# Performance work log

Measured on AMD Instinct MI355X. Metric: run time of the kernel, lower is better.

The kernel has to match this reference:

```python
import jax, jax.numpy as jnp
from jax import lax
import numpy as np

H = 256      # encoder_hidden
F = 256      # variance predictor filter_size
K = 3        # kernel_size
NBINS = 256  # variance_embedding n_bins
B, S, T = 64, 512, 2048


def conv1d(x, w, b, pad):
    # x: [B, L, Cin], w: [K, Cin, Cout] -> [B, L, Cout]
    y = lax.conv_general_dilated(x, w, window_strides=(1,), padding=[(pad, pad)],
                                 dimension_numbers=('NWC', 'WIO', 'NWC'))
    return y + b


def layer_norm(x, g, b, eps=1e-5):
    mu = jnp.mean(x, -1, keepdims=True)
    v = jnp.mean((x - mu) ** 2, -1, keepdims=True)
    return (x - mu) * lax.rsqrt(v + eps) * g + b


def predictor(x, mask, w1, b1, g1, be1, w2, b2, g2, be2, lw, lb):
    h = jax.nn.relu(conv1d(x, w1, b1, (K - 1) // 2))
    h = layer_norm(h, g1, be1)
    h = jax.nn.relu(conv1d(h, w2, b2, 1))  # padding=1 hardcoded in original conv1d_2
    h = layer_norm(h, g2, be2)
    out = (h @ lw + lb)[..., 0]            # [B, L]
    return jnp.where(mask, 0.0, out)       # masked_fill(mask, 0.0)


def setup_inputs():
    key = jax.random.key(0)
    ks = jax.random.split(key, 16)
    inp = {
        'x': jax.random.normal(ks[0], (B, S, H), jnp.float32),
        'pitch_target': jax.random.normal(ks[1], (B, S), jnp.float32),
        'energy_target': jax.random.normal(ks[2], (B, S), jnp.float32),
        'src_mask': jnp.zeros((B, S), bool),
        'duration': jax.random.randint(ks[3], (B, S), 0, 4, jnp.int32),
        'max_len': T,
    }
    i = 4
    for p in ['d', 'p', 'e']:
        inp[p + '_w1'] = jax.random.normal(ks[i], (K, H, F), jnp.float32) * 0.05; i += 1
        inp[p + '_b1'] = jnp.zeros((F,), jnp.float32)
        inp[p + '_g1'] = jnp.ones((F,), jnp.float32)
        inp[p + '_be1'] = jnp.zeros((F,), jnp.float32)
        inp[p + '_w2'] = jax.random.normal(ks[i], (K, F, F), jnp.float32) * 0.05; i += 1
        inp[p + '_b2'] = jnp.zeros((F,), jnp.float32)
        inp[p + '_g2'] = jnp.ones((F,), jnp.float32)
        inp[p + '_be2'] = jnp.zeros((F,), jnp.float32)
        inp[p + '_lw'] = jax.random.normal(ks[i], (F, 1), jnp.float32) * 0.05; i += 1
        inp[p + '_lb'] = jnp.zeros((1,), jnp.float32)
    inp['p_table'] = jax.random.normal(ks[i], (NBINS, H), jnp.float32) * 0.02; i += 1
    inp['e_table'] = jax.random.normal(ks[i], (NBINS, H), jnp.float32) * 0.02
    return inp


def reference(x, pitch_target, energy_target, src_mask, duration, max_len,
              d_w1, d_b1, d_g1, d_be1, d_w2, d_b2, d_g2, d_be2, d_lw, d_lb,
              p_w1, p_b1, p_g1, p_be1, p_w2, p_b2, p_g2, p_be2, p_lw, p_lb,
              e_w1, e_b1, e_g1, e_be1, e_w2, e_b2, e_g2, e_be2, e_lw, e_lb,
              p_table, e_table):
    # linear-quantized bins over the data range (stats.json min/max -> [-2, 2] for randn data)
    bins = jnp.linspace(-2.0, 2.0, NBINS - 1, dtype=jnp.float32)

    log_d_pred = predictor(x, src_mask, d_w1, d_b1, d_g1, d_be1, d_w2, d_b2, d_g2, d_be2, d_lw, d_lb)

    # phoneme-level pitch (training path: target given -> embed bucketized target)
    p_pred = predictor(x, src_mask, p_w1, p_b1, p_g1, p_be1, p_w2, p_b2, p_g2, p_be2, p_lw, p_lb)
    p_emb = p_table[jnp.searchsorted(bins, pitch_target, side='left')]  # torch.bucketize(right=False)
    x = x + p_emb

    # phoneme-level energy (predictor runs on x AFTER pitch embedding, as in original)
    e_pred = predictor(x, src_mask, e_w1, e_b1, e_g1, e_be1, e_w2, e_b2, e_g2, e_be2, e_lw, e_lb)
    e_emb = e_table[jnp.searchsorted(bins, energy_target, side='left')]
    x = x + e_emb

    # Length regulation: expand phoneme i duration[b, i] times, pad to max_len.
    cum = jnp.cumsum(duration, axis=1)                 # [B, S]
    mel_len = cum[:, -1]                               # [B]
    frames = jnp.arange(max_len)                       # [T]
    # frame t maps to first phoneme i with cum[i] > t
    idx = jax.vmap(lambda c: jnp.searchsorted(c, frames, side='right'))(cum)  # [B, T]
    idx = jnp.minimum(idx, duration.shape[1] - 1)
    mel = jnp.take_along_axis(x, idx[:, :, None], axis=1)                     # [B, T, H]
    valid = frames[None, :] < mel_len[:, None]
    mel = jnp.where(valid[:, :, None], mel, 0.0)       # zero-pad beyond mel_len

    d_rounded = duration
    return (mel, p_pred, e_pred, log_d_pred, d_rounded, mel_len)
```

## Files before the change

kernel.cpp:

```cpp
#include <hip/hip_runtime.h>
#include <cstdint>
#include <cstddef>


#define HH 256
#define SS 512
#define BB 64
#define TT 2048

typedef __bf16 bf16;
typedef __attribute__((ext_vector_type(8))) __bf16 bf16x8;
typedef __attribute__((ext_vector_type(4))) __bf16 bf16x4;
typedef __attribute__((ext_vector_type(4))) float f32x4;

static constexpr size_t WSZ  = (size_t)3 * HH * HH;
static constexpr size_t H1SZ = (size_t)BB * SS * HH;

__device__ __forceinline__ int swz(int r, int c) { return (r * HH + c) ^ ((r & 7) << 3); }

__device__ __forceinline__ float edge_val(int j) {
    const float step = 4.0f / 254.0f;
    if (j == 254) return 2.0f;
    return __fadd_rn(-2.0f, __fmul_rn((float)j, step));
}
__device__ __forceinline__ int bucket256(float v) {
    int lo = 0, hi = 255;
    while (lo < hi) {
        int mid = (lo + hi) >> 1;
        if (edge_val(mid) < v) lo = mid + 1; else hi = mid;
    }
    return lo;
}

__global__ void wt_pack(const float* __restrict__ w0, const float* __restrict__ w1,
                        const float* __restrict__ w2, const float* __restrict__ w3,
                        const float* __restrict__ w4, const float* __restrict__ w5,
                        bf16* __restrict__ wp) {
    const int cv = blockIdx.x / 3, k = blockIdx.x % 3;
    const float* wsel[6] = {w0, w1, w2, w3, w4, w5};
    const float* wk = wsel[cv] + (size_t)k * HH * HH;
    bf16* o = wp + ((size_t)(cv * 3 + k)) * HH * HH;
    for (int fb = 0; fb < 16; ++fb) {
        #pragma unroll
        for (int h = 0; h < 2; ++h) {
            const int idx  = threadIdx.x + 256 * h;
            const int kcb  = idx >> 6, lane = idx & 63;
            const int f    = fb * 16 + (lane & 15);
            const int c0   = kcb * 32 + (lane >> 4) * 8;
            bf16x8 v;
            #pragma unroll
            for (int j = 0; j < 8; ++j) v[j] = (bf16)wk[(size_t)(c0 + j) * HH + f];
            *(bf16x8*)(o + (((size_t)fb * 8 + kcb) * 64 + lane) * 8) = v;
        }
    }
}

struct Args3 {
    const float* bias[3];
    const float* g[3];
    const float* be[3];
    const float* lw[3];
    const float* lb[3];
    float*       out[3];
};

template <bool LIN>
__global__ __launch_bounds__(256, 3) void conv_all(
    const void* __restrict__ in,
    const float* __restrict__ tab,
    const float* __restrict__ tgt,
    const bf16* __restrict__ wpk,
    Args3 args,
    bf16* __restrict__ h1out,
    const uint8_t* __restrict__ mask)
{
    __shared__ alignas(16) bf16 tile[66 * HH];
    __shared__ float red_s[64][4], red_q[64][4];
    __shared__ float ln_m[64], ln_r[64];
    __shared__ int remb[66];

    const int tid    = threadIdx.x;
    const int pred   = blockIdx.x >> 9;
    const int within = blockIdx.x & 511;
    const int b      = within >> 3;
    const int s0     = (within & 7) * 64;
    const bool emb   = (!LIN) && (pred == 2);

    if (emb) {
        if (tid < 66) {
            int s = s0 - 1 + tid;
            remb[tid] = (s >= 0 && s < SS) ? bucket256(tgt[b * SS + s]) : 0;
        }
        __syncthreads();
    }

    if (!LIN) {
        const float* inb = (const float*)in + (size_t)b * SS * HH;
        for (int idx = tid; idx < 66 * 64; idx += 256) {
            const int r = idx >> 6, c4 = (idx & 63) << 2;
            const int s = s0 - 1 + r;
            float4 v = make_float4(0.f, 0.f, 0.f, 0.f);
            if (s >= 0 && s < SS) {
                v = *(const float4*)(inb + (size_t)s * HH + c4);
                if (emb) {
                    const float4 tv = *(const float4*)(tab + (size_t)remb[r] * HH + c4);
                    v.x += tv.x; v.y += tv.y; v.z += tv.z; v.w += tv.w;
                }
            }
            bf16x4 bv = {(bf16)v.x, (bf16)v.y, (bf16)v.z, (bf16)v.w};
            *(bf16x4*)&tile[swz(r, c4)] = bv;
        }
    } else {
        const bf16* inb = (const bf16*)in + (size_t)pred * H1SZ + (size_t)b * SS * HH;
        for (int idx = tid; idx < 66 * 32; idx += 256) {
            const int r = idx >> 5, c8 = (idx & 31) << 3;
            const int s = s0 - 1 + r;
            bf16x8 v = {};
            if (s >= 0 && s < SS) v = *(const bf16x8*)(inb + (size_t)s * HH + c8);
            *(bf16x8*)&tile[swz(r, c8)] = v;
        }
    }
    __syncthreads();

    const int lane = tid & 63;
    const int wv   = tid >> 6;
    const int ln15 = lane & 15;
    const int g8   = (lane >> 4) << 3;

    const bf16* wt = wpk + (size_t)(pred * 2 + (LIN ? 1 : 0)) * WSZ;

    f32x4 acc[4][4];
    #pragma unroll
    for (int nf = 0; nf < 4; ++nf) {
        const float bv = args.bias[pred][wv * 64 + nf * 16 + ln15];
        #pragma unroll
        for (int mf = 0; mf < 4; ++mf) acc[mf][nf] = f32x4{bv, bv, bv, bv};
    }

    bf16x8 a0[4], b0[4], a1[4], b1[4];

#define LOADSTEP(A_, B_, T_) do {                                              \
    const int k_ = (T_) >> 3, kcb_ = (T_) & 7;                                 \
    const int kc_ = kcb_ << 5;                                                 \
    const int ar_ = ln15 + k_;                                                 \
    _Pragma("unroll")                                                          \
    for (int mf_ = 0; mf_ < 4; ++mf_)                                          \
        A_[mf_] = *(const bf16x8*)&tile[swz(16 * mf_ + ar_, kc_ + g8)];        \
    const bf16* bp_ = wt + ((((size_t)k_ * 16 + wv * 4) * 8 + kcb_) << 9)      \
                         + (size_t)lane * 8;                                   \
    _Pragma("unroll")                                                          \
    for (int nf_ = 0; nf_ < 4; ++nf_)                                          \
        B_[nf_] = *(const bf16x8*)(bp_ + ((size_t)nf_ << 12));                 \
} while (0)

#define MFMASTEP(A_, B_) do {                                                  \
    _Pragma("unroll")                                                          \
    for (int mf_ = 0; mf_ < 4; ++mf_)                                          \
        _Pragma("unroll")                                                      \
        for (int nf_ = 0; nf_ < 4; ++nf_)                                      \
            acc[mf_][nf_] = __builtin_amdgcn_mfma_f32_16x16x32_bf16(           \
                A_[mf_], B_[nf_], acc[mf_][nf_], 0, 0, 0);                     \
} while (0)

    LOADSTEP(a0, b0, 0);
    #pragma unroll 1
    for (int t2 = 0; t2 < 11; ++t2) {
        const int t = 2 * t2;
        LOADSTEP(a1, b1, t + 1);
        MFMASTEP(a0, b0);
        LOADSTEP(a0, b0, t + 2);
        MFMASTEP(a1, b1);
    }
    LOADSTEP(a1, b1, 23);
    MFMASTEP(a0, b0);
    MFMASTEP(a1, b1);

#undef LOADSTEP
#undef MFMASTEP

    #pragma unroll
    for (int mf = 0; mf < 4; ++mf)
        #pragma unroll
        for (int nf = 0; nf < 4; ++nf)
            #pragma unroll
            for (int i = 0; i < 4; ++i)
                acc[mf][nf][i] = fmaxf(acc[mf][nf][i], 0.f);

    #pragma unroll
    for (int mf = 0; mf < 4; ++mf) {
        #pragma unroll
        for (int i = 0; i < 4; ++i) {
            float s = acc[mf][0][i] + acc[mf][1][i] + acc[mf][2][i] + acc[mf][3][i];
            float q = acc[mf][0][i] * acc[mf][0][i] + acc[mf][1][i] * acc[mf][1][i] +
                      acc[mf][2][i] * acc[mf][2][i] + acc[mf][3][i] * acc[mf][3][i];
            #pragma unroll
            for (int off = 1; off < 16; off <<= 1) {
                s += __shfl_xor(s, off);
                q += __shfl_xor(q, off);
            }
            if (ln15 == 0) {
                const int row = 16 * mf + (lane >> 4) * 4 + i;
                red_s[row][wv] = s;
                red_q[row][wv] = q;
            }
        }
    }
    __syncthreads();
    if (tid < 64) {
        const float s = red_s[tid][0] + red_s[tid][1] + red_s[tid][2] + red_s[tid][3];
        const float q = red_q[tid][0] + red_q[tid][1] + red_q[tid][2] + red_q[tid][3];
        const float mean = s * (1.f / 256.f);
        const float var  = q * (1.f / 256.f) - mean * mean;
        ln_m[tid] = mean;
        ln_r[tid] = rsqrtf(var + 1e-5f);
    }
    __syncthreads();

    float gv[4], bev[4];
    #pragma unroll
    for (int nf = 0; nf < 4; ++nf) {
        const int col = wv * 64 + nf * 16 + ln15;
        gv[nf]  = args.g[pred][col];
        bev[nf] = args.be[pred][col];
    }

    if (!LIN) {
        bf16* ob = h1out + (size_t)pred * H1SZ + ((size_t)(b * SS + s0)) * HH;
        #pragma unroll
        for (int mf = 0; mf < 4; ++mf) {
            #pragma unroll
            for (int i = 0; i < 4; ++i) {
                const int row = 16 * mf + (lane >> 4) * 4 + i;
                const float mean = ln_m[row], rs = ln_r[row];
                #pragma unroll
                for (int nf = 0; nf < 4; ++nf) {
                    const float o = (acc[mf][nf][i] - mean) * rs * gv[nf] + bev[nf];
                    ob[(size_t)row * HH + wv * 64 + nf * 16 + ln15] = (bf16)o;
                }
            }
        }
    } else {
        float lwv[4];
        #pragma unroll
        for (int nf = 0; nf < 4; ++nf) lwv[nf] = args.lw[pred][wv * 64 + nf * 16 + ln15];
        const float lb0 = args.lb[pred][0];
        #pragma unroll
        for (int mf = 0; mf < 4; ++mf) {
            #pragma unroll
            for (int i = 0; i < 4; ++i) {
                const int row = 16 * mf + (lane >> 4) * 4 + i;
                const float mean = ln_m[row], rs = ln_r[row];
                float t = 0.f;
                #pragma unroll
                for (int nf = 0; nf < 4; ++nf)
                    t += ((acc[mf][nf][i] - mean) * rs * gv[nf] + bev[nf]) * lwv[nf];
                #pragma unroll
                for (int off = 1; off < 16; off <<= 1) t += __shfl_xor(t, off);
                if (ln15 == 0) red_s[row][wv] = t;
            }
        }
        __syncthreads();
        if (tid < 64) {
            const int gr = b * SS + s0 + tid;
            const float dv = red_s[tid][0] + red_s[tid][1] + red_s[tid][2] + red_s[tid][3] + lb0;
            args.out[pred][gr] = mask[gr] ? 0.f : dv;
        }
    }
}

__global__ void dur_kernel(const int* __restrict__ dur, int* __restrict__ idxb,
                           int* __restrict__ mli,
                           float* __restrict__ drnd, float* __restrict__ mlen) {
    __shared__ int sb[SS];
    const int b = blockIdx.x, t = threadIdx.x;
    const int v = dur[b * SS + t];
    drnd[b * SS + t] = (float)v;
    sb[t] = v;
    __syncthreads();
    for (int off = 1; off < SS; off <<= 1) {
        const int add = (t >= off) ? sb[t - off] : 0;
        __syncthreads();
        sb[t] += add;
        __syncthreads();
    }
    const int hi = sb[t];
    const int lo = hi - v;
    for (int j = lo; j < hi; ++j) idxb[b * TT + j] = t;
    if (t == SS - 1) { mlen[b] = (float)hi; mli[b] = hi; }
}

__global__ __launch_bounds__(256) void gather_kernel(
    const float* __restrict__ x,
    const float* __restrict__ ptab, const float* __restrict__ pt,
    const float* __restrict__ etab, const float* __restrict__ et,
    const int* __restrict__ idxb, const int* __restrict__ mli,
    float* __restrict__ mel)
{
    const int lane = threadIdx.x & 63;
    for (int row = blockIdx.x * 4 + (threadIdx.x >> 6); row < BB * TT; row += 4096 * 4) {
        const int b = row >> 11;
        const int t = row & (TT - 1);
        float4 v = make_float4(0.f, 0.f, 0.f, 0.f);
        if (t < mli[b]) {
            const int idx = idxb[row];
            const size_t src = ((size_t)b * SS + idx) * HH + lane * 4;
            v = *(const float4*)(x + src);
            const int pb = bucket256(pt[b * SS + idx]);
            const int eb = bucket256(et[b * SS + idx]);
            const float4 pv = *(const float4*)(ptab + (size_t)pb * HH + lane * 4);
            const float4 ev = *(const float4*)(etab + (size_t)eb * HH + lane * 4);
            v.x += pv.x + ev.x; v.y += pv.y + ev.y; v.z += pv.z + ev.z; v.w += pv.w + ev.w;
        }
        *(float4*)(mel + (size_t)row * HH + lane * 4) = v;
    }
}

extern "C" void kernel_launch(void* const* d_in, const int* in_sizes, int n_in,
                              void* d_out, int out_size, void* d_ws, size_t ws_size,
                              hipStream_t stream) {
    (void)in_sizes; (void)n_in; (void)out_size; (void)ws_size;

    const float*   x      = (const float*)d_in[0];
    const float*   pitch  = (const float*)d_in[1];
    const float*   energy = (const float*)d_in[2];
    const uint8_t* mask   = (const uint8_t*)d_in[3];
    const int*     dur    = (const int*)d_in[4];
    const float*   ptab   = (const float*)d_in[36];
    const float*   etab   = (const float*)d_in[37];

    float* out = (float*)d_out;
    const size_t N_MEL = (size_t)BB * TT * HH;
    float* out_p  = out + N_MEL;
    float* out_e  = out_p + (size_t)BB * SS;
    float* out_ld = out_e + (size_t)BB * SS;
    float* out_dr = out_ld + (size_t)BB * SS;
    float* out_ml = out_dr + (size_t)BB * SS;

    bf16* wpk  = (bf16*)d_ws;
    int*  idxb = (int*)(wpk + 6 * WSZ);
    int*  mli  = idxb + (size_t)BB * TT;

    bf16* h1 = (bf16*)out;

    wt_pack<<<18, 256, 0, stream>>>(
        (const float*)d_in[6],  (const float*)d_in[10],
        (const float*)d_in[16], (const float*)d_in[20],
        (const float*)d_in[26], (const float*)d_in[30],
        wpk);
    dur_kernel<<<BB, SS, 0, stream>>>(dur, idxb, mli, out_dr, out_ml);

    Args3 a1 = {
        {(const float*)d_in[7],  (const float*)d_in[17], (const float*)d_in[27]},
        {(const float*)d_in[8],  (const float*)d_in[18], (const float*)d_in[28]},
        {(const float*)d_in[9],  (const float*)d_in[19], (const float*)d_in[29]},
        {nullptr, nullptr, nullptr}, {nullptr, nullptr, nullptr},
        {nullptr, nullptr, nullptr}
    };
    Args3 a2 = {
        {(const float*)d_in[11], (const float*)d_in[21], (const float*)d_in[31]},
        {(const float*)d_in[12], (const float*)d_in[22], (const float*)d_in[32]},
        {(const float*)d_in[13], (const float*)d_in[23], (const float*)d_in[33]},
        {(const float*)d_in[14], (const float*)d_in[24], (const float*)d_in[34]},
        {(const float*)d_in[15], (const float*)d_in[25], (const float*)d_in[35]},
        {out_ld, out_p, out_e}
    };

    conv_all<false><<<3 * 512, 256, 0, stream>>>(x, ptab, pitch, wpk, a1, h1, nullptr);
    conv_all<true ><<<3 * 512, 256, 0, stream>>>(h1, nullptr, nullptr, wpk, a2, nullptr, mask);

    gather_kernel<<<4096, 256, 0, stream>>>(x, ptab, pitch, etab, energy, idxb, mli, out);
}
```

Measured before the change: 164.3 us.

## Switch conv MFMA warp tiling to 2x2 layout with simple unrolled loop

Reassigns each wave from a 64-row by 64-column output slab to a 32-row by 128-column slab, halving LDS A-fragment reads but doubling per-wave weight fragment loads from global memory. The hand-written double-buffered load/MFMA pipeline is replaced by a plain loop unrolled by two, leaving overlap to the compiler. LayerNorm partial reductions now combine two column halves instead of four. This risks exposing more global-load latency and raising register pressure.

```diff
diff --git a/kernel.cpp b/kernel.cpp
--- a/kernel.cpp
+++ b/kernel.cpp
@@ -75,7 +75,7 @@
     const uint8_t* __restrict__ mask)
 {
     __shared__ alignas(16) bf16 tile[66 * HH];
-    __shared__ float red_s[64][4], red_q[64][4];
+    __shared__ float red_s[64][2], red_q[64][2];
     __shared__ float ln_m[64], ln_r[64];
     __shared__ int remb[66];
 
@@ -124,91 +124,75 @@
 
     const int lane = tid & 63;
     const int wv   = tid >> 6;
+    const int wr   = wv >> 1;
+    const int wc   = wv & 1;
     const int ln15 = lane & 15;
     const int g8   = (lane >> 4) << 3;
 
     const bf16* wt = wpk + (size_t)(pred * 2 + (LIN ? 1 : 0)) * WSZ;
 
-    f32x4 acc[4][4];
+    f32x4 acc[2][8];
     #pragma unroll
-    for (int nf = 0; nf < 4; ++nf) {
-        const float bv = args.bias[pred][wv * 64 + nf * 16 + ln15];
-        #pragma unroll
-        for (int mf = 0; mf < 4; ++mf) acc[mf][nf] = f32x4{bv, bv, bv, bv};
-    }
-
-    bf16x8 a0[4], b0[4], a1[4], b1[4];
-
-#define LOADSTEP(A_, B_, T_) do {                                              \
-    const int k_ = (T_) >> 3, kcb_ = (T_) & 7;                                 \
-    const int kc_ = kcb_ << 5;                                                 \
-    const int ar_ = ln15 + k_;                                                 \
-    _Pragma("unroll")                                                          \
-    for (int mf_ = 0; mf_ < 4; ++mf_)                                          \
-        A_[mf_] = *(const bf16x8*)&tile[swz(16 * mf_ + ar_, kc_ + g8)];        \
-    const bf16* bp_ = wt + ((((size_t)k_ * 16 + wv * 4) * 8 + kcb_) << 9)      \
-                         + (size_t)lane * 8;                                   \
-    _Pragma("unroll")                                                          \
-    for (int nf_ = 0; nf_ < 4; ++nf_)                                          \
-        B_[nf_] = *(const bf16x8*)(bp_ + ((size_t)nf_ << 12));                 \
-} while (0)
-
-#define MFMASTEP(A_, B_) do {                                                  \
-    _Pragma("unroll")                                                          \
-    for (int mf_ = 0; mf_ < 4; ++mf_)                                          \
-        _Pragma("unroll")                                                      \
-        for (int nf_ = 0; nf_ < 4; ++nf_)                                      \
-            acc[mf_][nf_] = __builtin_amdgcn_mfma_f32_16x16x32_bf16(           \
-                A_[mf_], B_[nf_], acc[mf_][nf_], 0, 0, 0);                     \
-} while (0)
-
-    LOADSTEP(a0, b0, 0);
-    #pragma unroll 1
-    for (int t2 = 0; t2 < 11; ++t2) {
-        const int t = 2 * t2;
-        LOADSTEP(a1, b1, t + 1);
-        MFMASTEP(a0, b0);
-        LOADSTEP(a0, b0, t + 2);
-        MFMASTEP(a1, b1);
-    }
-    LOADSTEP(a1, b1, 23);
-    MFMASTEP(a0, b0);
-    MFMASTEP(a1, b1);
-
-#undef LOADSTEP
-#undef MFMASTEP
+    for (int nf = 0; nf < 8; ++nf) {
+        const float bv = args.bias[pred][wc * 128 + nf * 16 + ln15];
+        #pragma unroll
+        for (int mf = 0; mf < 2; ++mf) acc[mf][nf] = f32x4{bv, bv, bv, bv};
+    }
+
+    #pragma unroll 2
+    for (int t = 0; t < 24; ++t) {
+        const int k = t >> 3, kcb = t & 7;
+        const int kc = kcb << 5;
+        bf16x8 a[2], bb[8];
+        #pragma unroll
+        for (int mf = 0; mf < 2; ++mf)
+            a[mf] = *(const bf16x8*)&tile[swz(32 * wr + 16 * mf + ln15 + k, kc + g8)];
+        const bf16* bp = wt + ((((size_t)k * 16 + wc * 8) * 8 + kcb) << 9) + (size_t)lane * 8;
+        #pragma unroll
+        for (int nf = 0; nf < 8; ++nf)
+            bb[nf] = *(const bf16x8*)(bp + ((size_t)nf << 12));
+        #pragma unroll
+        for (int mf = 0; mf < 2; ++mf)
+            #pragma unroll
+            for (int nf = 0; nf < 8; ++nf)
+                acc[mf][nf] = __builtin_amdgcn_mfma_f32_16x16x32_bf16(
+                    a[mf], bb[nf], acc[mf][nf], 0, 0, 0);
+    }
 
     #pragma unroll
-    for (int mf = 0; mf < 4; ++mf)
-        #pragma unroll
-        for (int nf = 0; nf < 4; ++nf)
+    for (int mf = 0; mf < 2; ++mf)
+        #pragma unroll
+        for (int nf = 0; nf < 8; ++nf)
             #pragma unroll
             for (int i = 0; i < 4; ++i)
                 acc[mf][nf][i] = fmaxf(acc[mf][nf][i], 0.f);
 
     #pragma unroll
-    for (int mf = 0; mf < 4; ++mf) {
+    for (int mf = 0; mf < 2; ++mf) {
         #pragma unroll
         for (int i = 0; i < 4; ++i) {
-            float s = acc[mf][0][i] + acc[mf][1][i] + acc[mf][2][i] + acc[mf][3][i];
-            float q = acc[mf][0][i] * acc[mf][0][i] + acc[mf][1][i] * acc[mf][1][i] +
-                      acc[mf][2][i] * acc[mf][2][i] + acc[mf][3][i] * acc[mf][3][i];
+            float s = 0.f, q = 0.f;
+            #pragma unroll
+            for (int nf = 0; nf < 8; ++nf) {
+                s += acc[mf][nf][i];
+                q += acc[mf][nf][i] * acc[mf][nf][i];
+            }
             #pragma unroll
             for (int off = 1; off < 16; off <<= 1) {
                 s += __shfl_xor(s, off);
                 q += __shfl_xor(q, off);
             }
             if (ln15 == 0) {
-                const int row = 16 * mf + (lane >> 4) * 4 + i;
-                red_s[row][wv] = s;
-                red_q[row][wv] = q;
+                const int row = 32 * wr + 16 * mf + (lane >> 4) * 4 + i;
+                red_s[row][wc] = s;
+                red_q[row][wc] = q;
             }
         }
     }
     __syncthreads();
     if (tid < 64) {
-        const float s = red_s[tid][0] + red_s[tid][1] + red_s[tid][2] + red_s[tid][3];
-        const float q = red_q[tid][0] + red_q[tid][1] + red_q[tid][2] + red_q[tid][3];
+        const float s = red_s[tid][0] + red_s[tid][1];
+        const float q = red_q[tid][0] + red_q[tid][1];
         const float mean = s * (1.f / 256.f);
         const float var  = q * (1.f / 256.f) - mean * mean;
         ln_m[tid] = mean;
@@ -216,10 +200,10 @@
     }
     __syncthreads();
 
-    float gv[4], bev[4];
+    float gv[8], bev[8];
     #pragma unroll
-    for (int nf = 0; nf < 4; ++nf) {
-        const int col = wv * 64 + nf * 16 + ln15;
+    for (int nf = 0; nf < 8; ++nf) {
+        const int col = wc * 128 + nf * 16 + ln15;
         gv[nf]  = args.g[pred][col];
         bev[nf] = args.be[pred][col];
     }
@@ -227,42 +211,42 @@
     if (!LIN) {
         bf16* ob = h1out + (size_t)pred * H1SZ + ((size_t)(b * SS + s0)) * HH;
         #pragma unroll
-        for (int mf = 0; mf < 4; ++mf) {
+        for (int mf = 0; mf < 2; ++mf) {
             #pragma unroll
             for (int i = 0; i < 4; ++i) {
-                const int row = 16 * mf + (lane >> 4) * 4 + i;
+                const int row = 32 * wr + 16 * mf + (lane >> 4) * 4 + i;
                 const float mean = ln_m[row], rs = ln_r[row];
                 #pragma unroll
-                for (int nf = 0; nf < 4; ++nf) {
+                for (int nf = 0; nf < 8; ++nf) {
                     const float o = (acc[mf][nf][i] - mean) * rs * gv[nf] + bev[nf];
-                    ob[(size_t)row * HH + wv * 64 + nf * 16 + ln15] = (bf16)o;
+                    ob[(size_t)row * HH + wc * 128 + nf * 16 + ln15] = (bf16)o;
                 }
             }
         }
     } else {
-        float lwv[4];
-        #pragma unroll
-        for (int nf = 0; nf < 4; ++nf) lwv[nf] = args.lw[pred][wv * 64 + nf * 16 + ln15];
+        float lwv[8];
+        #pragma unroll
+        for (int nf = 0; nf < 8; ++nf) lwv[nf] = args.lw[pred][wc * 128 + nf * 16 + ln15];
         const float lb0 = args.lb[pred][0];
         #pragma unroll
-        for (int mf = 0; mf < 4; ++mf) {
+        for (int mf = 0; mf < 2; ++mf) {
             #pragma unroll
             for (int i = 0; i < 4; ++i) {
-                const int row = 16 * mf + (lane >> 4) * 4 + i;
+                const int row = 32 * wr + 16 * mf + (lane >> 4) * 4 + i;
                 const float mean = ln_m[row], rs = ln_r[row];
                 float t = 0.f;
                 #pragma unroll
-                for (int nf = 0; nf < 4; ++nf)
+                for (int nf = 0; nf < 8; ++nf)
                     t += ((acc[mf][nf][i] - mean) * rs * gv[nf] + bev[nf]) * lwv[nf];
                 #pragma unroll
                 for (int off = 1; off < 16; off <<= 1) t += __shfl_xor(t, off);
-                if (ln15 == 0) red_s[row][wv] = t;
+                if (ln15 == 0) red_s[row][wc] = t;
             }
         }
         __syncthreads();
         if (tid < 64) {
             const int gr = b * SS + s0 + tid;
-            const float dv = red_s[tid][0] + red_s[tid][1] + red_s[tid][2] + red_s[tid][3] + lb0;
+            const float dv = red_s[tid][0] + red_s[tid][1] + lb0;
             args.out[pred][gr] = mask[gr] ? 0.f : dv;
         }
     }
```

Result: no change. 165.6 us (+0.8%).
